# Kernel tuning notes

Measured on AMD Instinct MI355X. Metric: run time of the kernel, lower is better.

Reference implementation:

```python
import jax, jax.numpy as jnp
import numpy as np

D_MODEL = 1024
D_FF = 8192
N_ELEM = 64            # d2 (elements per block)
D1 = D_FF // N_ELEM    # 128 block rows
BATCH = 2048


def setup_inputs() -> dict:
    key = jax.random.key(0)
    k1, k2, k3, k4, k5 = jax.random.split(key, 5)
    # xavier-uniform-like init for w1 (d_model, d_ff) -> view (d_model, d1, d2)
    bound1 = float(np.sqrt(6.0 / (D_MODEL + D_FF)))
    w1 = jax.random.uniform(k1, (D_MODEL, D1, N_ELEM), jnp.float32, -bound1, bound1)
    # w2 (d_ff, d_model) -> view (d2, d1, d_model); kernel_scaling=True multiplies by sqrt(d2)
    w2 = jax.random.uniform(k2, (N_ELEM, D1, D_MODEL), jnp.float32, -bound1, bound1)
    w2 = w2 * (N_ELEM ** 0.5)
    b2 = jax.random.normal(k3, (D_MODEL,), jnp.float32)
    x = jax.random.normal(k4, (BATCH, D_MODEL), jnp.float32)
    quant_mask = jax.random.randint(k5, (BATCH, D1), 0, N_ELEM, jnp.int32)
    return {"quant_mask": quant_mask, "x": x, "w1": w1, "w2": w2, "b2": b2}


def reference(quant_mask, x, w1, w2, b2):
    # predict-mode path of SparseFFMain (multiply_by_controller_output=False)
    d1 = w1.shape[1]
    w1p = jnp.transpose(w1, (1, 2, 0))   # (d1, d2, d_model)
    w2p = jnp.transpose(w2, (1, 0, 2))   # (d1, d2, d_model)
    rows = jnp.arange(d1)[None, :]        # (1, d1) broadcasts over batch
    # per-sample gathered expert sub-blocks: (B, d1, d_model)
    w = w1p[rows, quant_mask]
    v = w2p[rows, quant_mask]
    mid = jnp.einsum('bd,bjd->bj', x, w)   # (B, d1)
    relu = jax.nn.relu(mid)
    res = jnp.einsum('bj,bjd->bd', relu, v) + b2  # (B, d_model)
    return (quant_mask, res)
```

## Files before the change

### kernel.cpp

```cpp
#include <hip/hip_runtime.h>

#define D_MODEL 1024
#define D_FF    8192
#define N_ELEM  64
#define D1      128
#define BATCH   2048

typedef unsigned short u16;
typedef unsigned int   u32;

__device__ __forceinline__ float bflo(u32 u) {
    union { u32 i; float f; } c; c.i = u << 16; return c.f;
}
__device__ __forceinline__ float bfhi(u32 u) {
    union { u32 i; float f; } c; c.i = u & 0xffff0000u; return c.f;
}
__device__ __forceinline__ u16 f2bf(float f) {
    union { float f; u32 i; } c; c.f = f;
    u32 r = c.i + 0x7fff + ((c.i >> 16) & 1);
    return (u16)(r >> 16);
}

__global__ __launch_bounds__(256) void transpose_cast_w1(const float* __restrict__ w1,
                                                         u16* __restrict__ w1t) {
    __shared__ float tile[64][65];
    const int c0 = blockIdx.x * 64;
    const int d0 = blockIdx.y * 64;
    const int tx = threadIdx.x & 15;
    const int ty = threadIdx.x >> 4;

#pragma unroll
    for (int r = 0; r < 4; ++r) {
        const int row = ty * 4 + r;
        const float4 v = *(const float4*)(w1 + (size_t)(d0 + row) * D_FF + c0 + tx * 4);
        tile[row][tx * 4 + 0] = v.x;
        tile[row][tx * 4 + 1] = v.y;
        tile[row][tx * 4 + 2] = v.z;
        tile[row][tx * 4 + 3] = v.w;
    }
    __syncthreads();
#pragma unroll
    for (int r = 0; r < 4; ++r) {
        const int c = ty * 4 + r;
        ushort4 o;
        o.x = f2bf(tile[tx * 4 + 0][c]);
        o.y = f2bf(tile[tx * 4 + 1][c]);
        o.z = f2bf(tile[tx * 4 + 2][c]);
        o.w = f2bf(tile[tx * 4 + 3][c]);
        *(ushort4*)(w1t + (size_t)(c0 + c) * D_MODEL + d0 + tx * 4) = o;
    }
}

__global__ __launch_bounds__(256) void cast_w2(const float* __restrict__ w2,
                                               u16* __restrict__ w2b) {
    const size_t i = ((size_t)blockIdx.x * 256 + threadIdx.x) * 8;
    const float4 a = *(const float4*)(w2 + i);
    const float4 b = *(const float4*)(w2 + i + 4);
    ushort4 oa, ob;
    oa.x = f2bf(a.x); oa.y = f2bf(a.y); oa.z = f2bf(a.z); oa.w = f2bf(a.w);
    ob.x = f2bf(b.x); ob.y = f2bf(b.y); ob.z = f2bf(b.z); ob.w = f2bf(b.w);
    *(ushort4*)(w2b + i)     = oa;
    *(ushort4*)(w2b + i + 4) = ob;
}

__global__ __launch_bounds__(256) void sparse_ff_bf16(const int* __restrict__ mask,
                                                      const float* __restrict__ x,
                                                      const u16* __restrict__ w1t,
                                                      const u16* __restrict__ w2b,
                                                      const float* __restrict__ b2,
                                                      float* __restrict__ out) {
    __shared__ float x_lds[D_MODEL];
    __shared__ float relu_lds[D1];
    __shared__ int   m_lds[D1];
    __shared__ __align__(16) int   act_off[D1];
    __shared__ __align__(16) float act_r[D1];
    __shared__ int nact_s;

    const int b = blockIdx.x;
    const int t = threadIdx.x;
    const int wave = t >> 6;
    const int lane = t & 63;

    *(float4*)&x_lds[t * 4] = *(const float4*)(x + (size_t)b * D_MODEL + t * 4);
    if (t < D1) {
        const int mv = mask[b * D1 + t];
        m_lds[t] = mv;
        out[(size_t)b * D1 + t] = (float)mv;
    }
    __syncthreads();

    float xr[16];
    {
        const float4 a0 = *(const float4*)&x_lds[lane * 8];
        const float4 a1 = *(const float4*)&x_lds[lane * 8 + 4];
        const float4 b0 = *(const float4*)&x_lds[512 + lane * 8];
        const float4 b1 = *(const float4*)&x_lds[512 + lane * 8 + 4];
        xr[0]=a0.x; xr[1]=a0.y; xr[2]=a0.z; xr[3]=a0.w;
        xr[4]=a1.x; xr[5]=a1.y; xr[6]=a1.z; xr[7]=a1.w;
        xr[8]=b0.x; xr[9]=b0.y; xr[10]=b0.z; xr[11]=b0.w;
        xr[12]=b1.x; xr[13]=b1.y; xr[14]=b1.z; xr[15]=b1.w;
    }

    for (int jj = 0; jj < 32; jj += 4) {
        const int jbase = wave * 32 + jj;
        uint4 wa[4], wb[4];
#pragma unroll
        for (int q = 0; q < 4; ++q) {
            const int j = jbase + q;
            const u16* col = w1t + (size_t)(j * N_ELEM + m_lds[j]) * D_MODEL;
            wa[q] = *(const uint4*)(col + lane * 8);
            wb[q] = *(const uint4*)(col + 512 + lane * 8);
        }
#pragma unroll
        for (int q = 0; q < 4; ++q) {
            float acc = 0.f;
            acc = fmaf(bflo(wa[q].x), xr[0], acc);  acc = fmaf(bfhi(wa[q].x), xr[1], acc);
            acc = fmaf(bflo(wa[q].y), xr[2], acc);  acc = fmaf(bfhi(wa[q].y), xr[3], acc);
            acc = fmaf(bflo(wa[q].z), xr[4], acc);  acc = fmaf(bfhi(wa[q].z), xr[5], acc);
            acc = fmaf(bflo(wa[q].w), xr[6], acc);  acc = fmaf(bfhi(wa[q].w), xr[7], acc);
            acc = fmaf(bflo(wb[q].x), xr[8], acc);  acc = fmaf(bfhi(wb[q].x), xr[9], acc);
            acc = fmaf(bflo(wb[q].y), xr[10], acc); acc = fmaf(bfhi(wb[q].y), xr[11], acc);
            acc = fmaf(bflo(wb[q].z), xr[12], acc); acc = fmaf(bfhi(wb[q].z), xr[13], acc);
            acc = fmaf(bflo(wb[q].w), xr[14], acc); acc = fmaf(bfhi(wb[q].w), xr[15], acc);
#pragma unroll
            for (int off = 32; off; off >>= 1) acc += __shfl_down(acc, off);
            if (lane == 0) relu_lds[jbase + q] = fmaxf(acc, 0.f);
        }
    }
    __syncthreads();

    if (wave == 0) {
        const float rA = relu_lds[lane];
        const float rB = relu_lds[64 + lane];
        const unsigned long long bA = __ballot(rA > 0.f);
        const unsigned long long bB = __ballot(rB > 0.f);
        const unsigned long long lt = (1ull << lane) - 1ull;
        const int cntA = __popcll(bA);
        if (rA > 0.f) {
            const int p = __popcll(bA & lt);
            act_r[p] = rA;
            act_off[p] = (m_lds[lane] * D1 + lane) * D_MODEL;
        }
        if (rB > 0.f) {
            const int p = cntA + __popcll(bB & lt);
            act_r[p] = rB;
            act_off[p] = (m_lds[64 + lane] * D1 + 64 + lane) * D_MODEL;
        }
        if (lane == 0) nact_s = cntA + __popcll(bB);
    }
    __syncthreads();

    const int nact = nact_s;
    const int dm0 = t * 4;
    const float4 bv = *(const float4*)(b2 + dm0);
    float a0 = bv.x, a1 = bv.y, a2 = bv.z, a3 = bv.w;

    int i = 0;
    for (; i + 4 <= nact; i += 4) {
        const int4   o4 = *(const int4*)&act_off[i];
        const float4 r4 = *(const float4*)&act_r[i];
        const uint2 v0 = *(const uint2*)(w2b + o4.x + dm0);
        const uint2 v1 = *(const uint2*)(w2b + o4.y + dm0);
        const uint2 v2 = *(const uint2*)(w2b + o4.z + dm0);
        const uint2 v3 = *(const uint2*)(w2b + o4.w + dm0);
        a0 = fmaf(r4.x, bflo(v0.x), a0); a1 = fmaf(r4.x, bfhi(v0.x), a1);
        a2 = fmaf(r4.x, bflo(v0.y), a2); a3 = fmaf(r4.x, bfhi(v0.y), a3);
        a0 = fmaf(r4.y, bflo(v1.x), a0); a1 = fmaf(r4.y, bfhi(v1.x), a1);
        a2 = fmaf(r4.y, bflo(v1.y), a2); a3 = fmaf(r4.y, bfhi(v1.y), a3);
        a0 = fmaf(r4.z, bflo(v2.x), a0); a1 = fmaf(r4.z, bfhi(v2.x), a1);
        a2 = fmaf(r4.z, bflo(v2.y), a2); a3 = fmaf(r4.z, bfhi(v2.y), a3);
        a0 = fmaf(r4.w, bflo(v3.x), a0); a1 = fmaf(r4.w, bfhi(v3.x), a1);
        a2 = fmaf(r4.w, bflo(v3.y), a2); a3 = fmaf(r4.w, bfhi(v3.y), a3);
    }
    for (; i < nact; ++i) {
        const int   off = act_off[i];
        const float r   = act_r[i];
        const uint2 v = *(const uint2*)(w2b + off + dm0);
        a0 = fmaf(r, bflo(v.x), a0); a1 = fmaf(r, bfhi(v.x), a1);
        a2 = fmaf(r, bflo(v.y), a2); a3 = fmaf(r, bfhi(v.y), a3);
    }

    *(float4*)(out + (size_t)BATCH * D1 + (size_t)b * D_MODEL + dm0) =
        make_float4(a0, a1, a2, a3);
}

__global__ __launch_bounds__(256) void sparse_ff_f32_raw(const int* __restrict__ mask,
                                                         const float* __restrict__ x,
                                                         const float* __restrict__ w1,
                                                         const float* __restrict__ w2,
                                                         const float* __restrict__ b2,
                                                         float* __restrict__ out) {
    __shared__ float x_lds[D_MODEL];
    __shared__ float relu_lds[D1];
    __shared__ int   m_lds[D1];
    const int b = blockIdx.x, t = threadIdx.x;
    const int wave = t >> 6, lane = t & 63;
    *(float4*)&x_lds[t * 4] = *(const float4*)(x + (size_t)b * D_MODEL + t * 4);
    if (t < D1) {
        const int mv = mask[b * D1 + t];
        m_lds[t] = mv;
        out[(size_t)b * D1 + t] = (float)mv;
    }
    __syncthreads();
    for (int jj = 0; jj < 32; ++jj) {
        const int j = wave * 32 + jj;
        const int m = m_lds[j];
        float acc = 0.f;
#pragma unroll
        for (int c = 0; c < 16; ++c) {
            const int d = c * 64 + lane;
            acc = fmaf(w1[(size_t)d * D_FF + j * N_ELEM + m], x_lds[d], acc);
        }
#pragma unroll
        for (int off = 32; off; off >>= 1) acc += __shfl_down(acc, off);
        if (lane == 0) relu_lds[j] = fmaxf(acc, 0.f);
    }
    __syncthreads();
    const int dm0 = t * 4;
    const float4 bv = *(const float4*)(b2 + dm0);
    float a0 = bv.x, a1 = bv.y, a2 = bv.z, a3 = bv.w;
    for (int j = 0; j < D1; ++j) {
        const float r = relu_lds[j];
        if (r > 0.f) {
            const float4 wv = *(const float4*)(w2 + (size_t)(m_lds[j] * D1 + j) * D_MODEL + dm0);
            a0 = fmaf(r, wv.x, a0); a1 = fmaf(r, wv.y, a1);
            a2 = fmaf(r, wv.z, a2); a3 = fmaf(r, wv.w, a3);
        }
    }
    *(float4*)(out + (size_t)BATCH * D1 + (size_t)b * D_MODEL + dm0) =
        make_float4(a0, a1, a2, a3);
}

extern "C" void kernel_launch(void* const* d_in, const int* in_sizes, int n_in,
                              void* d_out, int out_size, void* d_ws, size_t ws_size,
                              hipStream_t stream) {
    const int*   mask = (const int*)d_in[0];
    const float* x    = (const float*)d_in[1];
    const float* w1   = (const float*)d_in[2];
    const float* w2   = (const float*)d_in[3];
    const float* b2   = (const float*)d_in[4];
    float* out = (float*)d_out;

    const size_t w1t_bytes = (size_t)D_FF * D_MODEL * sizeof(u16);
    const size_t w2b_bytes = (size_t)D_FF * D_MODEL * sizeof(u16);

    if (ws_size >= w1t_bytes + w2b_bytes) {
        u16* w1t = (u16*)d_ws;
        u16* w2b = (u16*)((char*)d_ws + w1t_bytes);
        transpose_cast_w1<<<dim3(D_FF / 64, D_MODEL / 64), 256, 0, stream>>>(w1, w1t);
        cast_w2<<<(D_FF * D_MODEL / 8) / 256, 256, 0, stream>>>(w2, w2b);
        sparse_ff_bf16<<<BATCH, 256, 0, stream>>>(mask, x, w1t, w2b, b2, out);
    } else {
        sparse_ff_f32_raw<<<BATCH, 256, 0, stream>>>(mask, x, w1, w2, b2, out);
    }
}
```

Baseline: 194.3 us.

## Split sparse FFN across j-tiles and batch tiles with atomic accumulation

The single per-sample kernel is replaced by a tiled kernel in which each block handles 8 samples and a 16-row slice of the 128 expert block rows. Each block does both the gather-dot and the relu-weighted w2 accumulation for its slice, then atomically adds its partial output rows. A separate init kernel writes the mask echo and the b2 bias first. The intent is more parallelism and better locality on the gathered weight rows, at the cost of many float atomics, an extra launch, nontemporal x loads, and an output summation order that is no longer fixed.

```diff
diff --git a/kernel.cpp b/kernel.cpp
--- a/kernel.cpp
+++ b/kernel.cpp
@@ -5,9 +5,13 @@
 #define N_ELEM  64
 #define D1      128
 #define BATCH   2048
+#define B_T     8
+#define NJT     8
+#define JT      16
 
 typedef unsigned short u16;
 typedef unsigned int   u32;
+typedef float f32x4 __attribute__((ext_vector_type(4)));
 
 __device__ __forceinline__ float bflo(u32 u) {
     union { u32 i; float f; } c; c.i = u << 16; return c.f;
@@ -19,6 +23,9 @@
     union { float f; u32 i; } c; c.f = f;
     u32 r = c.i + 0x7fff + ((c.i >> 16) & 1);
     return (u16)(r >> 16);
+}
+__device__ __forceinline__ f32x4 ntload4(const float* p) {
+    return __builtin_nontemporal_load((const f32x4*)p);
 }
 
 __global__ __launch_bounds__(256) void transpose_cast_w1(const float* __restrict__ w1,
@@ -28,7 +35,6 @@
     const int d0 = blockIdx.y * 64;
     const int tx = threadIdx.x & 15;
     const int ty = threadIdx.x >> 4;
-
 #pragma unroll
     for (int r = 0; r < 4; ++r) {
         const int row = ty * 4 + r;
@@ -63,125 +69,109 @@
     *(ushort4*)(w2b + i + 4) = ob;
 }
 
-__global__ __launch_bounds__(256) void sparse_ff_bf16(const int* __restrict__ mask,
-                                                      const float* __restrict__ x,
-                                                      const u16* __restrict__ w1t,
-                                                      const u16* __restrict__ w2b,
-                                                      const float* __restrict__ b2,
-                                                      float* __restrict__ out) {
-    __shared__ float x_lds[D_MODEL];
-    __shared__ float relu_lds[D1];
-    __shared__ int   m_lds[D1];
-    __shared__ __align__(16) int   act_off[D1];
-    __shared__ __align__(16) float act_r[D1];
-    __shared__ int nact_s;
-
+__global__ __launch_bounds__(256) void init_out(const int* __restrict__ mask,
+                                                const float* __restrict__ b2,
+                                                float* __restrict__ out) {
     const int b = blockIdx.x;
+    const int t = threadIdx.x;
+    if (t < D1) out[(size_t)b * D1 + t] = (float)mask[b * D1 + t];
+    const float4 bv = *(const float4*)(b2 + t * 4);
+    *(float4*)(out + (size_t)BATCH * D1 + (size_t)b * D_MODEL + t * 4) = bv;
+}
+
+__global__ __launch_bounds__(256) void sparse_ff_jt(const int* __restrict__ mask,
+                                                    const float* __restrict__ x,
+                                                    const u16* __restrict__ w1t,
+                                                    const u16* __restrict__ w2b,
+                                                    float* __restrict__ out) {
+    __shared__ float r_lds[B_T][JT];
+    __shared__ int   m_lds[B_T][JT];
+
+    const int jt = blockIdx.x & (NJT - 1);
+    const int b0 = (blockIdx.x >> 3) * B_T;
     const int t = threadIdx.x;
     const int wave = t >> 6;
     const int lane = t & 63;
 
-    *(float4*)&x_lds[t * 4] = *(const float4*)(x + (size_t)b * D_MODEL + t * 4);
-    if (t < D1) {
-        const int mv = mask[b * D1 + t];
-        m_lds[t] = mv;
-        out[(size_t)b * D1 + t] = (float)mv;
-    }
-    __syncthreads();
-
-    float xr[16];
-    {
-        const float4 a0 = *(const float4*)&x_lds[lane * 8];
-        const float4 a1 = *(const float4*)&x_lds[lane * 8 + 4];
-        const float4 b0 = *(const float4*)&x_lds[512 + lane * 8];
-        const float4 b1 = *(const float4*)&x_lds[512 + lane * 8 + 4];
-        xr[0]=a0.x; xr[1]=a0.y; xr[2]=a0.z; xr[3]=a0.w;
-        xr[4]=a1.x; xr[5]=a1.y; xr[6]=a1.z; xr[7]=a1.w;
-        xr[8]=b0.x; xr[9]=b0.y; xr[10]=b0.z; xr[11]=b0.w;
-        xr[12]=b1.x; xr[13]=b1.y; xr[14]=b1.z; xr[15]=b1.w;
-    }
-
-    for (int jj = 0; jj < 32; jj += 4) {
-        const int jbase = wave * 32 + jj;
-        uint4 wa[4], wb[4];
-#pragma unroll
-        for (int q = 0; q < 4; ++q) {
-            const int j = jbase + q;
-            const u16* col = w1t + (size_t)(j * N_ELEM + m_lds[j]) * D_MODEL;
-            wa[q] = *(const uint4*)(col + lane * 8);
-            wb[q] = *(const uint4*)(col + 512 + lane * 8);
-        }
-#pragma unroll
-        for (int q = 0; q < 4; ++q) {
-            float acc = 0.f;
-            acc = fmaf(bflo(wa[q].x), xr[0], acc);  acc = fmaf(bfhi(wa[q].x), xr[1], acc);
-            acc = fmaf(bflo(wa[q].y), xr[2], acc);  acc = fmaf(bfhi(wa[q].y), xr[3], acc);
-            acc = fmaf(bflo(wa[q].z), xr[4], acc);  acc = fmaf(bfhi(wa[q].z), xr[5], acc);
-            acc = fmaf(bflo(wa[q].w), xr[6], acc);  acc = fmaf(bfhi(wa[q].w), xr[7], acc);
-            acc = fmaf(bflo(wb[q].x), xr[8], acc);  acc = fmaf(bfhi(wb[q].x), xr[9], acc);
-            acc = fmaf(bflo(wb[q].y), xr[10], acc); acc = fmaf(bfhi(wb[q].y), xr[11], acc);
-            acc = fmaf(bflo(wb[q].z), xr[12], acc); acc = fmaf(bfhi(wb[q].z), xr[13], acc);
-            acc = fmaf(bflo(wb[q].w), xr[14], acc); acc = fmaf(bfhi(wb[q].w), xr[15], acc);
-#pragma unroll
-            for (int off = 32; off; off >>= 1) acc += __shfl_down(acc, off);
-            if (lane == 0) relu_lds[jbase + q] = fmaxf(acc, 0.f);
-        }
-    }
-    __syncthreads();
-
-    if (wave == 0) {
-        const float rA = relu_lds[lane];
-        const float rB = relu_lds[64 + lane];
-        const unsigned long long bA = __ballot(rA > 0.f);
-        const unsigned long long bB = __ballot(rB > 0.f);
-        const unsigned long long lt = (1ull << lane) - 1ull;
-        const int cntA = __popcll(bA);
-        if (rA > 0.f) {
-            const int p = __popcll(bA & lt);
-            act_r[p] = rA;
-            act_off[p] = (m_lds[lane] * D1 + lane) * D_MODEL;
-        }
-        if (rB > 0.f) {
-            const int p = cntA + __popcll(bB & lt);
-            act_r[p] = rB;
-            act_off[p] = (m_lds[64 + lane] * D1 + 64 + lane) * D_MODEL;
-        }
-        if (lane == 0) nact_s = cntA + __popcll(bB);
-    }
-    __syncthreads();
-
-    const int nact = nact_s;
-    const int dm0 = t * 4;
-    const float4 bv = *(const float4*)(b2 + dm0);
-    float a0 = bv.x, a1 = bv.y, a2 = bv.z, a3 = bv.w;
-
-    int i = 0;
-    for (; i + 4 <= nact; i += 4) {
-        const int4   o4 = *(const int4*)&act_off[i];
-        const float4 r4 = *(const float4*)&act_r[i];
-        const uint2 v0 = *(const uint2*)(w2b + o4.x + dm0);
-        const uint2 v1 = *(const uint2*)(w2b + o4.y + dm0);
-        const uint2 v2 = *(const uint2*)(w2b + o4.z + dm0);
-        const uint2 v3 = *(const uint2*)(w2b + o4.w + dm0);
-        a0 = fmaf(r4.x, bflo(v0.x), a0); a1 = fmaf(r4.x, bfhi(v0.x), a1);
-        a2 = fmaf(r4.x, bflo(v0.y), a2); a3 = fmaf(r4.x, bfhi(v0.y), a3);
-        a0 = fmaf(r4.y, bflo(v1.x), a0); a1 = fmaf(r4.y, bfhi(v1.x), a1);
-        a2 = fmaf(r4.y, bflo(v1.y), a2); a3 = fmaf(r4.y, bfhi(v1.y), a3);
-        a0 = fmaf(r4.z, bflo(v2.x), a0); a1 = fmaf(r4.z, bfhi(v2.x), a1);
-        a2 = fmaf(r4.z, bflo(v2.y), a2); a3 = fmaf(r4.z, bfhi(v2.y), a3);
-        a0 = fmaf(r4.w, bflo(v3.x), a0); a1 = fmaf(r4.w, bfhi(v3.x), a1);
-        a2 = fmaf(r4.w, bflo(v3.y), a2); a3 = fmaf(r4.w, bfhi(v3.y), a3);
-    }
-    for (; i < nact; ++i) {
-        const int   off = act_off[i];
-        const float r   = act_r[i];
-        const uint2 v = *(const uint2*)(w2b + off + dm0);
-        a0 = fmaf(r, bflo(v.x), a0); a1 = fmaf(r, bfhi(v.x), a1);
-        a2 = fmaf(r, bflo(v.y), a2); a3 = fmaf(r, bfhi(v.y), a3);
-    }
-
-    *(float4*)(out + (size_t)BATCH * D1 + (size_t)b * D_MODEL + dm0) =
-        make_float4(a0, a1, a2, a3);
+    if (t < B_T * JT) {
+        const int bi = t >> 4, jj = t & (JT - 1);
+        m_lds[bi][jj] = mask[(b0 + bi) * D1 + jt * JT + jj];
+    }
+    __syncthreads();
+
+#pragma unroll
+    for (int rep = 0; rep < 2; ++rep) {
+        const int bi = wave * 2 + rep;
+        const float* xrow = x + (size_t)(b0 + bi) * D_MODEL;
+        const f32x4 xa0 = ntload4(xrow + lane * 8);
+        const f32x4 xa1 = ntload4(xrow + lane * 8 + 4);
+        const f32x4 xb0 = ntload4(xrow + 512 + lane * 8);
+        const f32x4 xb1 = ntload4(xrow + 512 + lane * 8 + 4);
+
+        for (int jj = 0; jj < JT; jj += 2) {
+            const int j0 = jt * JT + jj;
+            const u16* c0 = w1t + (size_t)(j0 * N_ELEM + m_lds[bi][jj]) * D_MODEL;
+            const u16* c1 = w1t + (size_t)((j0 + 1) * N_ELEM + m_lds[bi][jj + 1]) * D_MODEL;
+            const uint4 a0 = *(const uint4*)(c0 + lane * 8);
+            const uint4 b0v = *(const uint4*)(c0 + 512 + lane * 8);
+            const uint4 a1 = *(const uint4*)(c1 + lane * 8);
+            const uint4 b1v = *(const uint4*)(c1 + 512 + lane * 8);
+
+            float s0 = 0.f, s1 = 0.f;
+            s0 = fmaf(bflo(a0.x), xa0.x, s0);  s0 = fmaf(bfhi(a0.x), xa0.y, s0);
+            s0 = fmaf(bflo(a0.y), xa0.z, s0);  s0 = fmaf(bfhi(a0.y), xa0.w, s0);
+            s0 = fmaf(bflo(a0.z), xa1.x, s0);  s0 = fmaf(bfhi(a0.z), xa1.y, s0);
+            s0 = fmaf(bflo(a0.w), xa1.z, s0);  s0 = fmaf(bfhi(a0.w), xa1.w, s0);
+            s0 = fmaf(bflo(b0v.x), xb0.x, s0); s0 = fmaf(bfhi(b0v.x), xb0.y, s0);
+            s0 = fmaf(bflo(b0v.y), xb0.z, s0); s0 = fmaf(bfhi(b0v.y), xb0.w, s0);
+            s0 = fmaf(bflo(b0v.z), xb1.x, s0); s0 = fmaf(bfhi(b0v.z), xb1.y, s0);
+            s0 = fmaf(bflo(b0v.w), xb1.z, s0); s0 = fmaf(bfhi(b0v.w), xb1.w, s0);
+
+            s1 = fmaf(bflo(a1.x), xa0.x, s1);  s1 = fmaf(bfhi(a1.x), xa0.y, s1);
+            s1 = fmaf(bflo(a1.y), xa0.z, s1);  s1 = fmaf(bfhi(a1.y), xa0.w, s1);
+            s1 = fmaf(bflo(a1.z), xa1.x, s1);  s1 = fmaf(bfhi(a1.z), xa1.y, s1);
+            s1 = fmaf(bflo(a1.w), xa1.z, s1);  s1 = fmaf(bfhi(a1.w), xa1.w, s1);
+            s1 = fmaf(bflo(b1v.x), xb0.x, s1); s1 = fmaf(bfhi(b1v.x), xb0.y, s1);
+            s1 = fmaf(bflo(b1v.y), xb0.z, s1); s1 = fmaf(bfhi(b1v.y), xb0.w, s1);
+            s1 = fmaf(bflo(b1v.z), xb1.x, s1); s1 = fmaf(bfhi(b1v.z), xb1.y, s1);
+            s1 = fmaf(bflo(b1v.w), xb1.z, s1); s1 = fmaf(bfhi(b1v.w), xb1.w, s1);
+
+#pragma unroll
+            for (int off = 32; off; off >>= 1) {
+                s0 += __shfl_down(s0, off);
+                s1 += __shfl_down(s1, off);
+            }
+            if (lane == 0) {
+                r_lds[bi][jj]     = fmaxf(s0, 0.f);
+                r_lds[bi][jj + 1] = fmaxf(s1, 0.f);
+            }
+        }
+    }
+    __syncthreads();
+
+    const int d0q = t * 4;
+    float* resb = out + (size_t)BATCH * D1;
+    for (int bi = 0; bi < B_T; ++bi) {
+        float a0 = 0.f, a1 = 0.f, a2 = 0.f, a3 = 0.f;
+        int any = 0;
+        for (int jj = 0; jj < JT; ++jj) {
+            const float r = r_lds[bi][jj];
+            if (r > 0.f) {
+                any = 1;
+                const int j = jt * JT + jj;
+                const uint2 v = *(const uint2*)(w2b + (size_t)(m_lds[bi][jj] * D1 + j) * D_MODEL + d0q);
+                a0 = fmaf(r, bflo(v.x), a0); a1 = fmaf(r, bfhi(v.x), a1);
+                a2 = fmaf(r, bflo(v.y), a2); a3 = fmaf(r, bfhi(v.y), a3);
+            }
+        }
+        if (any) {
+            float* p = resb + (size_t)(b0 + bi) * D_MODEL + d0q;
+            atomicAdd(p + 0, a0);
+            atomicAdd(p + 1, a1);
+            atomicAdd(p + 2, a2);
+            atomicAdd(p + 3, a3);
+        }
+    }
 }
 
 __global__ __launch_bounds__(256) void sparse_ff_f32_raw(const int* __restrict__ mask,
@@ -249,7 +239,8 @@
         u16* w2b = (u16*)((char*)d_ws + w1t_bytes);
         transpose_cast_w1<<<dim3(D_FF / 64, D_MODEL / 64), 256, 0, stream>>>(w1, w1t);
         cast_w2<<<(D_FF * D_MODEL / 8) / 256, 256, 0, stream>>>(w2, w2b);
-        sparse_ff_bf16<<<BATCH, 256, 0, stream>>>(mask, x, w1t, w2b, b2, out);
+        init_out<<<BATCH, 256, 0, stream>>>(mask, b2, out);
+        sparse_ff_jt<<<(BATCH / B_T) * NJT, 256, 0, stream>>>(mask, x, w1t, w2b, out);
     } else {
         sparse_ff_f32_raw<<<BATCH, 256, 0, stream>>>(mask, x, w1, w2, b2, out);
     }
```

New measurement: 386.8 us. +99.0%, slower.

## Split sparse FF over j-tiles with bf16 partials and a separate reduction

Applied to the files above, without the earlier changes.

Replaces the per-sample kernel with one that processes 8 samples by 16 block rows per workgroup. Each workgroup writes bf16 partial outputs to workspace, and a second kernel sums the partials with the bias. The aim is to improve L2 locality of the gathered w1/w2 rows, since each block touches only a slice of the weights. The cost is an extra launch, 32 MB of partial traffic, and lost precision from storing partials in bf16. The new path runs only if the workspace is large enough; otherwise the old paths remain.

```diff
diff --git a/kernel.cpp b/kernel.cpp
--- a/kernel.cpp
+++ b/kernel.cpp
@@ -5,9 +5,14 @@
 #define N_ELEM  64
 #define D1      128
 #define BATCH   2048
+#define B_T     8
+#define NJT     8
+#define JT      16
 
 typedef unsigned short u16;
 typedef unsigned int   u32;
+typedef float f32x4 __attribute__((ext_vector_type(4)));
+typedef short s16x4 __attribute__((ext_vector_type(4)));
 
 __device__ __forceinline__ float bflo(u32 u) {
     union { u32 i; float f; } c; c.i = u << 16; return c.f;
@@ -19,6 +24,9 @@
     union { float f; u32 i; } c; c.f = f;
     u32 r = c.i + 0x7fff + ((c.i >> 16) & 1);
     return (u16)(r >> 16);
+}
+__device__ __forceinline__ f32x4 ntload4(const float* p) {
+    return __builtin_nontemporal_load((const f32x4*)p);
 }
 
 __global__ __launch_bounds__(256) void transpose_cast_w1(const float* __restrict__ w1,
@@ -28,7 +36,6 @@
     const int d0 = blockIdx.y * 64;
     const int tx = threadIdx.x & 15;
     const int ty = threadIdx.x >> 4;
-
 #pragma unroll
     for (int r = 0; r < 4; ++r) {
         const int row = ty * 4 + r;
@@ -61,6 +68,117 @@
     ob.x = f2bf(b.x); ob.y = f2bf(b.y); ob.z = f2bf(b.z); ob.w = f2bf(b.w);
     *(ushort4*)(w2b + i)     = oa;
     *(ushort4*)(w2b + i + 4) = ob;
+}
+
+__global__ __launch_bounds__(256) void sparse_ff_jt(const int* __restrict__ mask,
+                                                    const float* __restrict__ x,
+                                                    const u16* __restrict__ w1t,
+                                                    const u16* __restrict__ w2b,
+                                                    u16* __restrict__ part) {
+    __shared__ float r_lds[B_T][JT];
+    __shared__ int   m_lds[B_T][JT];
+
+    const int jt = blockIdx.x & (NJT - 1);
+    const int b0 = (blockIdx.x >> 3) * B_T;
+    const int t = threadIdx.x;
+    const int wave = t >> 6;
+    const int lane = t & 63;
+
+    if (t < B_T * JT) {
+        const int bi = t >> 4, jj = t & (JT - 1);
+        m_lds[bi][jj] = mask[(b0 + bi) * D1 + jt * JT + jj];
+    }
+    __syncthreads();
+
+#pragma unroll
+    for (int rep = 0; rep < 2; ++rep) {
+        const int bi = wave * 2 + rep;
+        const float* xrow = x + (size_t)(b0 + bi) * D_MODEL;
+        const f32x4 xa0 = ntload4(xrow + lane * 8);
+        const f32x4 xa1 = ntload4(xrow + lane * 8 + 4);
+        const f32x4 xb0 = ntload4(xrow + 512 + lane * 8);
+        const f32x4 xb1 = ntload4(xrow + 512 + lane * 8 + 4);
+
+        for (int jj = 0; jj < JT; jj += 2) {
+            const int j0 = jt * JT + jj;
+            const u16* c0 = w1t + (size_t)(j0 * N_ELEM + m_lds[bi][jj]) * D_MODEL;
+            const u16* c1 = w1t + (size_t)((j0 + 1) * N_ELEM + m_lds[bi][jj + 1]) * D_MODEL;
+            const uint4 a0 = *(const uint4*)(c0 + lane * 8);
+            const uint4 b0v = *(const uint4*)(c0 + 512 + lane * 8);
+            const uint4 a1 = *(const uint4*)(c1 + lane * 8);
+            const uint4 b1v = *(const uint4*)(c1 + 512 + lane * 8);
+
+            float s0 = 0.f, s1 = 0.f;
+            s0 = fmaf(bflo(a0.x), xa0.x, s0);  s0 = fmaf(bfhi(a0.x), xa0.y, s0);
+            s0 = fmaf(bflo(a0.y), xa0.z, s0);  s0 = fmaf(bfhi(a0.y), xa0.w, s0);
+            s0 = fmaf(bflo(a0.z), xa1.x, s0);  s0 = fmaf(bfhi(a0.z), xa1.y, s0);
+            s0 = fmaf(bflo(a0.w), xa1.z, s0);  s0 = fmaf(bfhi(a0.w), xa1.w, s0);
+            s0 = fmaf(bflo(b0v.x), xb0.x, s0); s0 = fmaf(bfhi(b0v.x), xb0.y, s0);
+            s0 = fmaf(bflo(b0v.y), xb0.z, s0); s0 = fmaf(bfhi(b0v.y), xb0.w, s0);
+            s0 = fmaf(bflo(b0v.z), xb1.x, s0); s0 = fmaf(bfhi(b0v.z), xb1.y, s0);
+            s0 = fmaf(bflo(b0v.w), xb1.z, s0); s0 = fmaf(bfhi(b0v.w), xb1.w, s0);
+
+            s1 = fmaf(bflo(a1.x), xa0.x, s1);  s1 = fmaf(bfhi(a1.x), xa0.y, s1);
+            s1 = fmaf(bflo(a1.y), xa0.z, s1);  s1 = fmaf(bfhi(a1.y), xa0.w, s1);
+            s1 = fmaf(bflo(a1.z), xa1.x, s1);  s1 = fmaf(bfhi(a1.z), xa1.y, s1);
+            s1 = fmaf(bflo(a1.w), xa1.z, s1);  s1 = fmaf(bfhi(a1.w), xa1.w, s1);
+            s1 = fmaf(bflo(b1v.x), xb0.x, s1); s1 = fmaf(bfhi(b1v.x), xb0.y, s1);
+            s1 = fmaf(bflo(b1v.y), xb0.z, s1); s1 = fmaf(bfhi(b1v.y), xb0.w, s1);
+            s1 = fmaf(bflo(b1v.z), xb1.x, s1); s1 = fmaf(bfhi(b1v.z), xb1.y, s1);
+            s1 = fmaf(bflo(b1v.w), xb1.z, s1); s1 = fmaf(bfhi(b1v.w), xb1.w, s1);
+
+#pragma unroll
+            for (int off = 32; off; off >>= 1) {
+                s0 += __shfl_down(s0, off);
+                s1 += __shfl_down(s1, off);
+            }
+            if (lane == 0) {
+                r_lds[bi][jj]     = fmaxf(s0, 0.f);
+                r_lds[bi][jj + 1] = fmaxf(s1, 0.f);
+            }
+        }
+    }
+    __syncthreads();
+
+    const int d0q = t * 4;
+    for (int bi = 0; bi < B_T; ++bi) {
+        float a0 = 0.f, a1 = 0.f, a2 = 0.f, a3 = 0.f;
+        for (int jj = 0; jj < JT; ++jj) {
+            const float r = r_lds[bi][jj];
+            if (r > 0.f) {
+                const int j = jt * JT + jj;
+                const uint2 v = *(const uint2*)(w2b + (size_t)(m_lds[bi][jj] * D1 + j) * D_MODEL + d0q);
+                a0 = fmaf(r, bflo(v.x), a0); a1 = fmaf(r, bfhi(v.x), a1);
+                a2 = fmaf(r, bflo(v.y), a2); a3 = fmaf(r, bfhi(v.y), a3);
+            }
+        }
+        s16x4 o;
+        o.x = (short)f2bf(a0); o.y = (short)f2bf(a1);
+        o.z = (short)f2bf(a2); o.w = (short)f2bf(a3);
+        u16* pp = part + ((size_t)jt * BATCH + (b0 + bi)) * D_MODEL + d0q;
+        __builtin_nontemporal_store(o, (s16x4*)pp);
+    }
+}
+
+__global__ __launch_bounds__(256) void reduce_partials(const int* __restrict__ mask,
+                                                       const float* __restrict__ b2,
+                                                       const u16* __restrict__ part,
+                                                       float* __restrict__ out) {
+    const int b = blockIdx.x;
+    const int t = threadIdx.x;
+    if (t < D1) out[(size_t)b * D1 + t] = (float)mask[b * D1 + t];
+
+    const int d0 = t * 4;
+    const float4 bv = *(const float4*)(b2 + d0);
+    float a0 = bv.x, a1 = bv.y, a2 = bv.z, a3 = bv.w;
+#pragma unroll
+    for (int jt = 0; jt < NJT; ++jt) {
+        const uint2 v = *(const uint2*)(part + ((size_t)jt * BATCH + b) * D_MODEL + d0);
+        a0 += bflo(v.x); a1 += bfhi(v.x);
+        a2 += bflo(v.y); a3 += bfhi(v.y);
+    }
+    *(float4*)(out + (size_t)BATCH * D1 + (size_t)b * D_MODEL + d0) =
+        make_float4(a0, a1, a2, a3);
 }
 
 __global__ __launch_bounds__(256) void sparse_ff_bf16(const int* __restrict__ mask,
@@ -154,7 +272,6 @@
     const int dm0 = t * 4;
     const float4 bv = *(const float4*)(b2 + dm0);
     float a0 = bv.x, a1 = bv.y, a2 = bv.z, a3 = bv.w;
-
     int i = 0;
     for (; i + 4 <= nact; i += 4) {
         const int4   o4 = *(const int4*)&act_off[i];
@@ -179,7 +296,6 @@
         a0 = fmaf(r, bflo(v.x), a0); a1 = fmaf(r, bfhi(v.x), a1);
         a2 = fmaf(r, bflo(v.y), a2); a3 = fmaf(r, bfhi(v.y), a3);
     }
-
     *(float4*)(out + (size_t)BATCH * D1 + (size_t)b * D_MODEL + dm0) =
         make_float4(a0, a1, a2, a3);
 }
@@ -241,10 +357,19 @@
     const float* b2   = (const float*)d_in[4];
     float* out = (float*)d_out;
 
-    const size_t w1t_bytes = (size_t)D_FF * D_MODEL * sizeof(u16);
-    const size_t w2b_bytes = (size_t)D_FF * D_MODEL * sizeof(u16);
-
-    if (ws_size >= w1t_bytes + w2b_bytes) {
+    const size_t w1t_bytes  = (size_t)D_FF * D_MODEL * sizeof(u16);
+    const size_t w2b_bytes  = (size_t)D_FF * D_MODEL * sizeof(u16);
+    const size_t part_bytes = (size_t)NJT * BATCH * D_MODEL * sizeof(u16);
+
+    if (ws_size >= w1t_bytes + w2b_bytes + part_bytes) {
+        u16* w1t  = (u16*)d_ws;
+        u16* w2b  = (u16*)((char*)d_ws + w1t_bytes);
+        u16* part = (u16*)((char*)d_ws + w1t_bytes + w2b_bytes);
+        transpose_cast_w1<<<dim3(D_FF / 64, D_MODEL / 64), 256, 0, stream>>>(w1, w1t);
+        cast_w2<<<(D_FF * D_MODEL / 8) / 256, 256, 0, stream>>>(w2, w2b);
+        sparse_ff_jt<<<(BATCH / B_T) * NJT, 256, 0, stream>>>(mask, x, w1t, w2b, part);
+        reduce_partials<<<BATCH, 256, 0, stream>>>(mask, b2, part, out);
+    } else if (ws_size >= w1t_bytes + w2b_bytes) {
         u16* w1t = (u16*)d_ws;
         u16* w2b = (u16*)((char*)d_ws + w1t_bytes);
         transpose_cast_w1<<<dim3(D_FF / 64, D_MODEL / 64), 256, 0, stream>>>(w1, w1t);
```

Measured after the change: 183.3 us. 1.06x faster.
